# Kernel tuning notes

Hardware: AMD Instinct MI355X
Metric: run time of the kernel (lower is better)

The kernel has to match this reference:

```python
import jax, jax.numpy as jnp
import numpy as np

N = 300000   # nodes (src == target, full-graph layer)
E = 4000000  # edges
I = 128      # in_channels
O = 64       # out_channels
R = 7        # num_edge_types
T = 4        # num_node_types


def setup_inputs() -> dict:
    key = jax.random.key(0)
    ks = jax.random.split(key, 7)
    x = jax.random.normal(ks[0], (N, I), dtype=jnp.float32)
    edge_index = jax.random.randint(ks[1], (2, E), 0, N, dtype=jnp.int32)
    edge_type = jax.random.randint(ks[2], (E,), 0, R, dtype=jnp.int32)
    node_type = jax.random.randint(ks[3], (N,), 0, T, dtype=jnp.int32)
    scale = 1.0 / np.sqrt(I).astype(np.float32)
    W_rel = jax.random.normal(ks[4], (R, I, O), dtype=jnp.float32) * scale
    W_root = jax.random.normal(ks[5], (T, I, O), dtype=jnp.float32) * scale
    b_root = jnp.zeros((T, O), dtype=jnp.float32)
    return {"x": x, "edge_index": edge_index, "edge_type": edge_type,
            "node_type": node_type, "W_rel": W_rel, "W_root": W_root,
            "b_root": b_root}


def reference(x, edge_index, edge_type, node_type, W_rel, W_root, b_root):
    # RGCNConv: out = sum_r scatter_mean_r(W_r @ x[src]) + root_lin[node_type](x)
    n, r = x.shape[0], W_rel.shape[0]
    src, dst = edge_index[0], edge_index[1]

    # Per-relation transform of all source features: [R, N, O]
    h = jnp.einsum('ni,rio->rno', x, W_rel)
    # Gather per-edge messages with relation-dependent weights: [E, O]
    msg = h[edge_type, src]

    # Per-(dst node, relation) mean: scatter-mean within each relation, then sum.
    seg = dst * r + edge_type                       # combined segment key in [0, N*R)
    ones = jnp.ones(edge_type.shape, dtype=x.dtype)
    cnt = jax.ops.segment_sum(ones, seg, num_segments=n * r)  # [N*R]
    inv = 1.0 / jnp.maximum(cnt, 1.0)
    out = jax.ops.segment_sum(msg * inv[seg][:, None], dst, num_segments=n)  # [N, O]

    # Root linear per node type: out[mask_t] += x[mask_t] @ W_root[t] + b_root[t]
    root = jnp.einsum('ni,tio->tno', x, W_root) + b_root[:, None, :]  # [T, N, O]
    out = out + root[node_type, jnp.arange(n)]
    return out
```

## Files before the change

### kernel.cpp

```cpp
#include <hip/hip_runtime.h>
#include <stdint.h>

#define N_NODES 300000
#define N_EDGES 4000000
#define IC 128
#define OC 64
#define NREL 7
#define NTYP 4
#define NRELT 11
#define NGRP (N_NODES / 4)
#define AS 136
#define SCAN_CHUNK 8192

typedef __attribute__((ext_vector_type(8))) short short8;
typedef __attribute__((ext_vector_type(4))) float f32x4;

__device__ __forceinline__ uint32_t f32_to_bf16_rne(float f) {
    uint32_t b = __float_as_uint(f);
    return (b + 0x7fffu + ((b >> 16) & 1u)) >> 16;
}
__device__ __forceinline__ uint32_t pack_bf16(float lo, float hi) {
    return f32_to_bf16_rne(lo) | (f32_to_bf16_rne(hi) << 16);
}

__global__ void k_cvt_w(const float* __restrict__ Wrel, const float* __restrict__ Wroot,
                        uint16_t* __restrict__ Wt) {
    int i = blockIdx.x * blockDim.x + threadIdx.x;
    int rel = i >> 13, rem = i & 8191, o = rem >> 7, k = rem & 127;
    float v = (rel < NREL) ? Wrel[(rel * IC + k) * OC + o]
                           : Wroot[((rel - NREL) * IC + k) * OC + o];
    Wt[i] = (uint16_t)f32_to_bf16_rne(v);
}

__global__ void k_cvt_x(const float* __restrict__ x, uint16_t* __restrict__ xh) {
    size_t i = (size_t)blockIdx.x * blockDim.x + threadIdx.x;
    const float4* x4 = (const float4*)x;
    float4 u = x4[i * 2], w = x4[i * 2 + 1];
    uint4 pk;
    pk.x = pack_bf16(u.x, u.y); pk.y = pack_bf16(u.z, u.w);
    pk.z = pack_bf16(w.x, w.y); pk.w = pack_bf16(w.z, w.w);
    ((uint4*)xh)[i] = pk;
}

__global__ void k_hist(const int* __restrict__ ei, int* __restrict__ deg) {
    int i = blockIdx.x * 256 + threadIdx.x;
    if (i >= N_EDGES / 4) return;
    int4 d = ((const int4*)(ei + N_EDGES))[i];
    atomicAdd(&deg[d.x >> 2], 1);
    atomicAdd(&deg[d.y >> 2], 1);
    atomicAdd(&deg[d.z >> 2], 1);
    atomicAdd(&deg[d.w >> 2], 1);
}

__global__ void k_scan1(const int* __restrict__ deg, int* __restrict__ offs,
                        int* __restrict__ bsum) {
    __shared__ int s[1024];
    int t = threadIdx.x;
    size_t base = (size_t)blockIdx.x * SCAN_CHUNK + (size_t)t * 8;
    int v[8];
    if (base + 7 < NGRP) {
        int4 u0 = *(const int4*)(deg + base), u1 = *(const int4*)(deg + base + 4);
        v[0] = u0.x; v[1] = u0.y; v[2] = u0.z; v[3] = u0.w;
        v[4] = u1.x; v[5] = u1.y; v[6] = u1.z; v[7] = u1.w;
    } else {
        #pragma unroll
        for (int j = 0; j < 8; ++j) v[j] = (base + j < NGRP) ? deg[base + j] : 0;
    }
    int run = 0, pre[8];
    #pragma unroll
    for (int j = 0; j < 8; ++j) { pre[j] = run; run += v[j]; }
    s[t] = run; __syncthreads();
    for (int d = 1; d < 1024; d <<= 1) {
        int add = (t >= d) ? s[t - d] : 0;
        __syncthreads();
        s[t] += add;
        __syncthreads();
    }
    int excl = s[t] - run;
    if (base + 7 < NGRP) {
        int4 o0 = {excl + pre[0], excl + pre[1], excl + pre[2], excl + pre[3]};
        int4 o1 = {excl + pre[4], excl + pre[5], excl + pre[6], excl + pre[7]};
        *(int4*)(offs + base) = o0; *(int4*)(offs + base + 4) = o1;
    } else {
        for (int j = 0; j < 8; ++j) if (base + j < NGRP) offs[base + j] = excl + pre[j];
    }
    if (t == 1023) bsum[blockIdx.x] = s[1023];
}

__global__ void k_scan2(int* __restrict__ bsum, int nblk) {
    __shared__ int s[1024];
    int t = threadIdx.x;
    int carry = 0;
    for (int c0 = 0; c0 < nblk; c0 += 1024) {
        int i = c0 + t;
        int v = (i < nblk) ? bsum[i] : 0;
        s[t] = v; __syncthreads();
        for (int d = 1; d < 1024; d <<= 1) {
            int add = (t >= d) ? s[t - d] : 0;
            __syncthreads();
            s[t] += add;
            __syncthreads();
        }
        if (i < nblk) bsum[i] = carry + s[t] - v;
        int tot = s[1023];
        __syncthreads();
        carry += tot;
    }
}

__global__ void k_scan3(const int* __restrict__ offs, const int* __restrict__ bsum,
                        int* __restrict__ cur, int* __restrict__ offsW) {
    int i = blockIdx.x * 256 + threadIdx.x;
    if (i < NGRP) {
        int v = offs[i] + bsum[i / SCAN_CHUNK];
        cur[i] = v;
        offsW[i] = v;
    }
    if (i == 0) offsW[NGRP] = N_EDGES;
}

__global__ void k_scatter(const int* __restrict__ ei, const int* __restrict__ et,
                          int* __restrict__ cur, int* __restrict__ sorted) {
    int i = blockIdx.x * 256 + threadIdx.x;
    if (i >= N_EDGES / 4) return;
    int4 sv = ((const int4*)ei)[i];
    int4 dv = ((const int4*)(ei + N_EDGES))[i];
    int4 rv = ((const int4*)et)[i];
    { int pos = atomicAdd(&cur[dv.x >> 2], 1); sorted[pos] = sv.x | (rv.x << 19) | ((dv.x & 3) << 22); }
    { int pos = atomicAdd(&cur[dv.y >> 2], 1); sorted[pos] = sv.y | (rv.y << 19) | ((dv.y & 3) << 22); }
    { int pos = atomicAdd(&cur[dv.z >> 2], 1); sorted[pos] = sv.z | (rv.z << 19) | ((dv.z & 3) << 22); }
    { int pos = atomicAdd(&cur[dv.w >> 2], 1); sorted[pos] = sv.w | (rv.w << 19) | ((dv.w & 3) << 22); }
}

__global__ __launch_bounds__(256, 5)
void k_main(const uint16_t* __restrict__ xh, const uint16_t* __restrict__ Wt,
            const int* __restrict__ offsW, const int* __restrict__ sorted,
            const int* __restrict__ node_type, const float* __restrict__ b_root,
            float* __restrict__ out) {
    __shared__ uint16_t A[NREL * 16 * AS];
    __shared__ int nt16[16];
    int t = threadIdx.x, lane = t & 63, wave = t >> 6;
    int d0 = blockIdx.x * 16;
    if (t < 16) nt16[t] = node_type[d0 + t];
    uint32_t* Pk = (uint32_t*)A;
    int w4 = wave * 4;

    int g = blockIdx.x * 4 + wave;
    int mybase = __builtin_amdgcn_readfirstlane(offsW[g]);
    int myend  = __builtin_amdgcn_readfirstlane(offsW[g + 1]);
    int L = myend - mybase;
    if (L > 192) L = 192;

    int u0 = (lane < L)       ? sorted[mybase + lane]       : 0;
    int u1 = (64 + lane < L)  ? sorted[mybase + 64 + lane]  : 0;
    int u2 = (128 + lane < L) ? sorted[mybase + 128 + lane] : 0;

    int* sbuf = (int*)A + wave * 256;
    int* cnts = (int*)A + 1024 + wave * 32;
    if (lane < 32) cnts[lane] = 0;
    __syncthreads();
    int k0s = 0, k1s = 0, k2s = 0, rk0 = -1, rk1 = -1, rk2 = -1;
    if (lane < L)       { k0s = ((u0 >> 22) & 3) * 7 + ((u0 >> 19) & 7); rk0 = atomicAdd(&cnts[k0s], 1); }
    if (64 + lane < L)  { k1s = ((u1 >> 22) & 3) * 7 + ((u1 >> 19) & 7); rk1 = atomicAdd(&cnts[k1s], 1); }
    if (128 + lane < L) { k2s = ((u2 >> 22) & 3) * 7 + ((u2 >> 19) & 7); rk2 = atomicAdd(&cnts[k2s], 1); }
    __syncthreads();
    int c = (lane < 28) ? cnts[lane] : 0;
    int ps = c;
    #pragma unroll
    for (int d = 1; d < 32; d <<= 1) { int uu = __shfl_up(ps, d); if (lane >= d) ps += uu; }
    int start = ps - c;
    if (lane < 28) cnts[lane] = start;
    __syncthreads();
    if (rk0 >= 0) sbuf[cnts[k0s] + rk0] = u0;
    if (rk1 >= 0) sbuf[cnts[k1s] + rk1] = u1;
    if (rk2 >= 0) sbuf[cnts[k2s] + rk2] = u2;
    __syncthreads();
    int rec0 = (lane < L)       ? sbuf[lane]       : 0;
    int rec1 = (64 + lane < L)  ? sbuf[64 + lane]  : 0;
    int rec2 = (128 + lane < L) ? sbuf[128 + lane] : 0;
    __syncthreads();

    #pragma unroll
    for (int s = 0; s < 28; ++s) {
        int row = ((s % 7) * 16 + w4 + s / 7) * 68;
        Pk[row + lane] = 0u;
    }

    int e4 = lane >> 4;
    int l15_16 = (lane & 15) << 4;
    int idxt = lane & 0x3C;
    const char* xb = (const char*)xh;
    const uint32_t* xl = (const uint32_t*)xh + lane;

    float a0 = 0.f, a1 = 0.f;
    int aseg = -1, runStart = 0, arow = 0;

    int4 ring[16];
    #pragma unroll
    for (int s = 0; s < 16; ++s) {
        if (4 * s < L) {
            int pe = __builtin_amdgcn_ds_bpermute((4 * s + e4) << 2, rec0);
            uint32_t src = min((uint32_t)(pe & 0x7FFFF), (uint32_t)(N_NODES - 1));
            ring[s] = *(const int4*)(xb + (src << 8) + l15_16);
        }
    }

    int Lf = (L < 128) ? L : 128;
    for (int b0 = 0; b0 < Lf; b0 += 64) {
        #pragma unroll
        for (int s = 0; s < 16; ++s) {
            int b = b0 + 4 * s;
            if (b < Lf) {
                int rsel = (b < 64) ? rec0 : rec1;
                #pragma unroll
                for (int m = 0; m < 4; ++m) {
                    int k = b + m;
                    if (k < Lf) {
                        int p = __builtin_amdgcn_readlane(rsel, k & 63);
                        int seg = ((p >> 22) & 3) * 7 + ((p >> 19) & 7);
                        if (seg != aseg) {
                            if (aseg >= 0) {
                                float inv = 1.0f / (float)(k - runStart);
                                Pk[arow + lane] = pack_bf16(a0 * inv, a1 * inv);
                                a0 = 0.f; a1 = 0.f;
                            }
                            aseg = seg; runStart = k;
                            arow = (((p >> 19) & 7) * 16 + w4 + ((p >> 22) & 3)) * 68;
                        }
                        int q0 = __builtin_amdgcn_ds_bpermute(idxt + 64 * m, ring[s].x);
                        int q1 = __builtin_amdgcn_ds_bpermute(idxt + 64 * m, ring[s].y);
                        int q2 = __builtin_amdgcn_ds_bpermute(idxt + 64 * m, ring[s].z);
                        int q3 = __builtin_amdgcn_ds_bpermute(idxt + 64 * m, ring[s].w);
                        int t0 = (lane & 1) ? q1 : q0;
                        int t1 = (lane & 1) ? q3 : q2;
                        uint32_t u = (uint32_t)((lane & 2) ? t1 : t0);
                        a0 += __uint_as_float(u << 16);
                        a1 += __uint_as_float(u & 0xffff0000u);
                    }
                }
                int bn = b + 64;
                if (bn < Lf) {
                    int pe = __builtin_amdgcn_ds_bpermute(((bn & 63) + e4) << 2, rec1);
                    uint32_t src = min((uint32_t)(pe & 0x7FFFF), (uint32_t)(N_NODES - 1));
                    ring[s] = *(const int4*)(xb + (src << 8) + l15_16);
                }
            }
        }
    }
    for (int k = 128; k < L; ++k) {
        int p = __builtin_amdgcn_readlane(rec2, k - 128);
        int seg = ((p >> 22) & 3) * 7 + ((p >> 19) & 7);
        if (seg != aseg) {
            if (aseg >= 0) {
                float inv = 1.0f / (float)(k - runStart);
                Pk[arow + lane] = pack_bf16(a0 * inv, a1 * inv);
                a0 = 0.f; a1 = 0.f;
            }
            aseg = seg; runStart = k;
            arow = (((p >> 19) & 7) * 16 + w4 + ((p >> 22) & 3)) * 68;
        }
        uint32_t src = min((uint32_t)(p & 0x7FFFF), (uint32_t)(N_NODES - 1));
        uint32_t u = xl[(size_t)src * 64];
        a0 += __uint_as_float(u << 16);
        a1 += __uint_as_float(u & 0xffff0000u);
    }
    if (aseg >= 0) {
        float inv = 1.0f / (float)(L - runStart);
        Pk[arow + lane] = pack_bf16(a0 * inv, a1 * inv);
    }
    __syncthreads();

    int n = lane & 15, quad = lane >> 4;
    const uint16_t* Wb = Wt + (size_t)(wave * 16 + n) * 128;
    f32x4 cc = {0.f, 0.f, 0.f, 0.f};
    for (int rel = 0; rel < NREL; ++rel) {
        #pragma unroll
        for (int kb = 0; kb < 4; ++kb) {
            short8 af = *(const short8*)&A[(rel * 16 + n) * AS + kb * 32 + quad * 8];
            short8 bf = *(const short8*)&Wb[rel * 8192 + kb * 32 + quad * 8];
            cc = __builtin_amdgcn_mfma_f32_16x16x32_bf16(af, bf, cc, 0, 0, 0);
        }
    }
    short8 axk[4];
    const uint16_t* xr = xh + (size_t)(d0 + n) * 128;
    #pragma unroll
    for (int kb = 0; kb < 4; ++kb)
        axk[kb] = *(const short8*)(xr + kb * 32 + quad * 8);
    int myNt = nt16[n];
    const short8 z8 = {0, 0, 0, 0, 0, 0, 0, 0};
    #pragma unroll
    for (int tt = 0; tt < NTYP; ++tt) {
        #pragma unroll
        for (int kb = 0; kb < 4; ++kb) {
            short8 am = (myNt == tt) ? axk[kb] : z8;
            short8 bf = *(const short8*)&Wb[(NREL + tt) * 8192 + kb * 32 + quad * 8];
            cc = __builtin_amdgcn_mfma_f32_16x16x32_bf16(am, bf, cc, 0, 0, 0);
        }
    }

    int o = wave * 16 + n;
    #pragma unroll
    for (int rg = 0; rg < 4; ++rg) {
        int m = quad * 4 + rg;
        out[(size_t)(d0 + m) * 64 + o] = cc[rg] + b_root[nt16[m] * 64 + o];
    }
}

extern "C" void kernel_launch(void* const* d_in, const int* in_sizes, int n_in,
                              void* d_out, int out_size, void* d_ws, size_t ws_size,
                              hipStream_t stream) {
    const float* x      = (const float*)d_in[0];
    const int*   ei     = (const int*)d_in[1];
    const int*   etype  = (const int*)d_in[2];
    const int*   ntype  = (const int*)d_in[3];
    const float* Wrel   = (const float*)d_in[4];
    const float* Wroot  = (const float*)d_in[5];
    const float* broot  = (const float*)d_in[6];
    float* out = (float*)d_out;

    char* ws = (char*)d_ws;
    size_t p = 0;
    auto take = [&](size_t bytes) { size_t r = p; p += (bytes + 255) & ~(size_t)255; return r; };
    uint16_t* Wt     = (uint16_t*)(ws + take((size_t)NRELT * OC * IC * 2));
    int*      sorted = (int*)(ws + take((size_t)N_EDGES * 4));
    int*      offsW  = (int*)(ws + take((size_t)(NGRP + 1) * 4));
    int*      bsum   = (int*)(ws + take(16384));
    size_t    xbase  = take((size_t)N_NODES * IC * 2);
    uint16_t* xh     = (uint16_t*)(ws + xbase);
    int*      deg    = (int*)(ws + xbase);
    int*      offs   = (int*)(ws + xbase + (512 << 10));
    int*      cur    = (int*)(ws + xbase + (1024 << 10));
    (void)ws_size; (void)n_in; (void)in_sizes; (void)out_size;

    const int SCAN_BLKS = (NGRP + SCAN_CHUNK - 1) / SCAN_CHUNK;

    k_cvt_w<<<(NRELT * OC * IC) / 256, 256, 0, stream>>>(Wrel, Wroot, Wt);
    hipMemsetAsync(deg, 0, (size_t)NGRP * 4, stream);
    k_hist<<<(N_EDGES / 4 + 255) / 256, 256, 0, stream>>>(ei, deg);
    k_scan1<<<SCAN_BLKS, 1024, 0, stream>>>(deg, offs, bsum);
    k_scan2<<<1, 1024, 0, stream>>>(bsum, SCAN_BLKS);
    k_scan3<<<(NGRP + 255) / 256, 256, 0, stream>>>(offs, bsum, cur, offsW);
    k_scatter<<<(N_EDGES / 4 + 255) / 256, 256, 0, stream>>>(ei, etype, cur, sorted);
    k_cvt_x<<<(N_NODES * IC / 8) / 256, 256, 0, stream>>>(x, xh);
    k_main<<<N_NODES / 16, 256, 0, stream>>>(xh, Wt, offsW, sorted, ntype, broot, out);
}
```

Baseline: 1.284 ms.

## Replace atomic edge scatter with two-level bucket partition and local fine sort

The per-edge global atomic scatter into destination-group slots is replaced by a two-pass partition. First, edges are split into coarse 1024-node buckets using per-block shared histograms and a cross-block scan, and written out in coalesced runs. Then each bucket is sorted into per-group order inside shared memory. This aims to remove random global atomics and scattered 4-byte stores, at the cost of extra kernels, another pass over the edge array, and an overflow path for buckets larger than the shared buffer. Records now carry extra high bits for the local group id.

```diff
diff --git a/kernel.cpp b/kernel.cpp
--- a/kernel.cpp
+++ b/kernel.cpp
@@ -9,6 +9,10 @@
 #define NTYP 4
 #define NRELT 11
 #define NGRP (N_NODES / 4)
+#define NBKT 293
+#define PBLK 8192
+#define PBLKS ((N_EDGES + PBLK - 1) / PBLK)
+#define FCAP 16384
 #define AS 136
 #define SCAN_CHUNK 8192
 
@@ -42,14 +46,26 @@
     ((uint4*)xh)[i] = pk;
 }
 
-__global__ void k_hist(const int* __restrict__ ei, int* __restrict__ deg) {
-    int i = blockIdx.x * 256 + threadIdx.x;
-    if (i >= N_EDGES / 4) return;
-    int4 d = ((const int4*)(ei + N_EDGES))[i];
-    atomicAdd(&deg[d.x >> 2], 1);
-    atomicAdd(&deg[d.y >> 2], 1);
-    atomicAdd(&deg[d.z >> 2], 1);
-    atomicAdd(&deg[d.w >> 2], 1);
+__global__ __launch_bounds__(1024) void k_cnt1(const int* __restrict__ ei,
+                                               int* __restrict__ deg, int* __restrict__ cntB) {
+    __shared__ int h[NBKT];
+    int t = threadIdx.x;
+    for (int i = t; i < NBKT; i += 1024) h[i] = 0;
+    __syncthreads();
+    const int4* d4 = (const int4*)(ei + N_EDGES);
+    int i4 = blockIdx.x * (PBLK / 4) + t;
+    #pragma unroll
+    for (int j = 0; j < 2; ++j, i4 += 1024) {
+        if (i4 < N_EDGES / 4) {
+            int4 d = d4[i4];
+            atomicAdd(&h[d.x >> 10], 1); atomicAdd(&deg[d.x >> 2], 1);
+            atomicAdd(&h[d.y >> 10], 1); atomicAdd(&deg[d.y >> 2], 1);
+            atomicAdd(&h[d.z >> 10], 1); atomicAdd(&deg[d.z >> 2], 1);
+            atomicAdd(&h[d.w >> 10], 1); atomicAdd(&deg[d.w >> 2], 1);
+        }
+    }
+    __syncthreads();
+    for (int i = t; i < NBKT; i += 1024) cntB[i * PBLKS + blockIdx.x] = h[i];
 }
 
 __global__ void k_scan1(const int* __restrict__ deg, int* __restrict__ offs,
@@ -109,27 +125,122 @@
 }
 
 __global__ void k_scan3(const int* __restrict__ offs, const int* __restrict__ bsum,
-                        int* __restrict__ cur, int* __restrict__ offsW) {
+                        int* __restrict__ offsW) {
     int i = blockIdx.x * 256 + threadIdx.x;
-    if (i < NGRP) {
-        int v = offs[i] + bsum[i / SCAN_CHUNK];
-        cur[i] = v;
-        offsW[i] = v;
-    }
+    if (i < NGRP) offsW[i] = offs[i] + bsum[i / SCAN_CHUNK];
     if (i == 0) offsW[NGRP] = N_EDGES;
 }
 
-__global__ void k_scatter(const int* __restrict__ ei, const int* __restrict__ et,
-                          int* __restrict__ cur, int* __restrict__ sorted) {
-    int i = blockIdx.x * 256 + threadIdx.x;
-    if (i >= N_EDGES / 4) return;
-    int4 sv = ((const int4*)ei)[i];
-    int4 dv = ((const int4*)(ei + N_EDGES))[i];
-    int4 rv = ((const int4*)et)[i];
-    { int pos = atomicAdd(&cur[dv.x >> 2], 1); sorted[pos] = sv.x | (rv.x << 19) | ((dv.x & 3) << 22); }
-    { int pos = atomicAdd(&cur[dv.y >> 2], 1); sorted[pos] = sv.y | (rv.y << 19) | ((dv.y & 3) << 22); }
-    { int pos = atomicAdd(&cur[dv.z >> 2], 1); sorted[pos] = sv.z | (rv.z << 19) | ((dv.z & 3) << 22); }
-    { int pos = atomicAdd(&cur[dv.w >> 2], 1); sorted[pos] = sv.w | (rv.w << 19) | ((dv.w & 3) << 22); }
+__global__ __launch_bounds__(512) void k_scanB(int* __restrict__ cntB,
+                                               const int* __restrict__ offsW) {
+    __shared__ int s[512];
+    int b = blockIdx.x, t = threadIdx.x;
+    int v = (t < PBLKS) ? cntB[b * PBLKS + t] : 0;
+    s[t] = v; __syncthreads();
+    for (int d = 1; d < 512; d <<= 1) {
+        int add = (t >= d) ? s[t - d] : 0;
+        __syncthreads();
+        s[t] += add;
+        __syncthreads();
+    }
+    if (t < PBLKS) cntB[b * PBLKS + t] = s[t] - v + offsW[b * 256];
+}
+
+__global__ __launch_bounds__(1024) void k_part(const int* __restrict__ ei,
+                                               const int* __restrict__ et,
+                                               const int* __restrict__ cntB,
+                                               int* __restrict__ sorted) {
+    __shared__ int hist[NBKT + 1];
+    __shared__ int tmp[1024];
+    __shared__ int rbuf[PBLK];
+    int t = threadIdx.x, blk = blockIdx.x;
+    for (int i = t; i < NBKT + 1; i += 1024) hist[i] = 0;
+    __syncthreads();
+    const int4* s4 = (const int4*)ei;
+    const int4* d4 = (const int4*)(ei + N_EDGES);
+    const int4* r4 = (const int4*)et;
+    int rec[8], pk[8];
+    int i4 = blk * (PBLK / 4) + t;
+    #pragma unroll
+    for (int j = 0; j < 2; ++j, i4 += 1024) {
+        int base = j * 4;
+        if (i4 < N_EDGES / 4) {
+            int4 sv = s4[i4], dv = d4[i4], rv = r4[i4];
+            int dd[4] = {dv.x, dv.y, dv.z, dv.w};
+            int ss[4] = {sv.x, sv.y, sv.z, sv.w};
+            int rr[4] = {rv.x, rv.y, rv.z, rv.w};
+            #pragma unroll
+            for (int m = 0; m < 4; ++m) {
+                int d = dd[m], b = d >> 10;
+                rec[base + m] = ss[m] | (rr[m] << 19) | ((d & 3) << 22) | (((d >> 2) & 255) << 24);
+                int r = atomicAdd(&hist[b], 1);
+                pk[base + m] = (b << 16) | r;
+            }
+        } else {
+            #pragma unroll
+            for (int m = 0; m < 4; ++m) pk[base + m] = -1;
+        }
+    }
+    __syncthreads();
+    int v = (t < NBKT) ? hist[t] : 0;
+    tmp[t] = v; __syncthreads();
+    for (int d = 1; d < 1024; d <<= 1) {
+        int add = (t >= d) ? tmp[t - d] : 0;
+        __syncthreads();
+        tmp[t] += add;
+        __syncthreads();
+    }
+    int total = tmp[1023];
+    if (t < NBKT) hist[t] = tmp[t] - v;
+    if (t == 0) hist[NBKT] = total;
+    __syncthreads();
+    #pragma unroll
+    for (int j = 0; j < 8; ++j) {
+        if (pk[j] >= 0) rbuf[hist[pk[j] >> 16] + (pk[j] & 0xFFFF)] = rec[j];
+    }
+    __syncthreads();
+    int wave = t >> 6, lane = t & 63;
+    for (int bi = wave; bi < NBKT; bi += 16) {
+        int s0 = hist[bi], s1 = hist[bi + 1];
+        int go = cntB[bi * PBLKS + blk];
+        for (int j = s0 + lane; j < s1; j += 64)
+            sorted[go + (j - s0)] = rbuf[j];
+    }
+}
+
+__global__ __launch_bounds__(1024) void k_fine(int* __restrict__ sorted,
+                                               const int* __restrict__ offsW,
+                                               int* __restrict__ scratch) {
+    __shared__ int ob[FCAP];
+    __shared__ int go[257];
+    __shared__ int gc[256];
+    int t = threadIdx.x, b = blockIdx.x;
+    int g0 = b * 256;
+    int ng = min(256, NGRP - g0);
+    int base = offsW[g0];
+    for (int i = t; i <= ng; i += 1024) go[i] = offsW[g0 + i] - base;
+    for (int i = t; i < 256; i += 1024) gc[i] = 0;
+    __syncthreads();
+    int n = go[ng];
+    if (n <= FCAP) {
+        for (int i = t; i < n; i += 1024) {
+            int rec = sorted[base + i];
+            int gl = (rec >> 24) & 255;
+            int r = atomicAdd(&gc[gl], 1);
+            ob[go[gl] + r] = rec;
+        }
+        __syncthreads();
+        for (int i = t; i < n; i += 1024) sorted[base + i] = ob[i];
+    } else {
+        for (int i = t; i < n; i += 1024) scratch[base + i] = sorted[base + i];
+        __syncthreads();
+        for (int i = t; i < n; i += 1024) {
+            int rec = scratch[base + i];
+            int gl = (rec >> 24) & 255;
+            int r = atomicAdd(&gc[gl], 1);
+            sorted[base + go[gl] + r] = rec;
+        }
+    }
 }
 
 __global__ __launch_bounds__(256, 5)
@@ -297,7 +408,6 @@
             cc = __builtin_amdgcn_mfma_f32_16x16x32_bf16(am, bf, cc, 0, 0, 0);
         }
     }
-
     int o = wave * 16 + n;
     #pragma unroll
     for (int rg = 0; rg < 4; ++rg) {
@@ -326,21 +436,24 @@
     int*      offsW  = (int*)(ws + take((size_t)(NGRP + 1) * 4));
     int*      bsum   = (int*)(ws + take(16384));
     size_t    xbase  = take((size_t)N_NODES * IC * 2);
-    uint16_t* xh     = (uint16_t*)(ws + xbase);
-    int*      deg    = (int*)(ws + xbase);
-    int*      offs   = (int*)(ws + xbase + (512 << 10));
-    int*      cur    = (int*)(ws + xbase + (1024 << 10));
+    uint16_t* xh      = (uint16_t*)(ws + xbase);
+    int*      deg     = (int*)(ws + xbase);
+    int*      offs    = (int*)(ws + xbase + (512 << 10));
+    int*      cntB    = (int*)(ws + xbase + (1024 << 10));
+    int*      scratch = (int*)(ws + xbase + (2048 << 10));
     (void)ws_size; (void)n_in; (void)in_sizes; (void)out_size;
 
     const int SCAN_BLKS = (NGRP + SCAN_CHUNK - 1) / SCAN_CHUNK;
 
     k_cvt_w<<<(NRELT * OC * IC) / 256, 256, 0, stream>>>(Wrel, Wroot, Wt);
     hipMemsetAsync(deg, 0, (size_t)NGRP * 4, stream);
-    k_hist<<<(N_EDGES / 4 + 255) / 256, 256, 0, stream>>>(ei, deg);
+    k_cnt1<<<PBLKS, 1024, 0, stream>>>(ei, deg, cntB);
     k_scan1<<<SCAN_BLKS, 1024, 0, stream>>>(deg, offs, bsum);
     k_scan2<<<1, 1024, 0, stream>>>(bsum, SCAN_BLKS);
-    k_scan3<<<(NGRP + 255) / 256, 256, 0, stream>>>(offs, bsum, cur, offsW);
-    k_scatter<<<(N_EDGES / 4 + 255) / 256, 256, 0, stream>>>(ei, etype, cur, sorted);
+    k_scan3<<<(NGRP + 255) / 256, 256, 0, stream>>>(offs, bsum, offsW);
+    k_scanB<<<NBKT, 512, 0, stream>>>(cntB, offsW);
+    k_part<<<PBLKS, 1024, 0, stream>>>(ei, etype, cntB, sorted);
+    k_fine<<<NBKT, 1024, 0, stream>>>(sorted, offsW, scratch);
     k_cvt_x<<<(N_NODES * IC / 8) / 256, 256, 0, stream>>>(x, xh);
     k_main<<<N_NODES / 16, 256, 0, stream>>>(xh, Wt, offsW, sorted, ntype, broot, out);
 }
```

Measured after the change: 1.041 ms. 1.23x faster.
